# Performance work log

Hardware: AMD Instinct MI355X
Metric: run time of the kernel (lower is better)

## Reference

```python
import jax, jax.numpy as jnp
import numpy as np

N_NODES = 100000
NEG_SLOPE = 0.2  # DGL GATConv default


def gat_layer(x, W, al, ar, src, dst):
    # x: [N, F_in], W: [F_in, H*D], al/ar: [H, D]
    H, D = al.shape
    f = (x @ W).reshape(-1, H, D)                      # [N, H, D]
    el = jnp.einsum('nhd,hd->nh', f, al)               # src attn term
    er = jnp.einsum('nhd,hd->nh', f, ar)               # dst attn term
    e = jax.nn.leaky_relu(el[src] + er[dst], NEG_SLOPE)  # [E, H]
    # segment softmax over incoming edges of each dst node
    m = jax.ops.segment_max(e, dst, num_segments=N_NODES)
    m = jnp.where(jnp.isfinite(m), m, jnp.zeros_like(m))  # isolated nodes -> -inf guard
    ex = jnp.exp(e - m[dst])                           # [E, H]
    s = jax.ops.segment_sum(ex, dst, num_segments=N_NODES)
    alpha = ex / (s[dst] + 1e-9)                       # [E, H]
    msg = f[src] * alpha[:, :, None]                   # [E, H, D]
    out = jax.ops.segment_sum(msg, dst, num_segments=N_NODES)  # [N, H, D]
    return out.reshape(N_NODES, H * D)


def setup_inputs() -> dict:
    key = jax.random.key(0)
    ks = jax.random.split(key, 12)
    x = jax.random.normal(ks[0], (N_NODES, 128), dtype=jnp.float32)
    edge_index = jax.random.randint(ks[1], (2, 1600000), 0, N_NODES, dtype=jnp.int32)
    sc = 0.05
    W0 = jax.random.normal(ks[2], (128, 128), dtype=jnp.float32) * sc
    al0 = jax.random.normal(ks[3], (4, 32), dtype=jnp.float32) * sc
    ar0 = jax.random.normal(ks[4], (4, 32), dtype=jnp.float32) * sc
    W1 = jax.random.normal(ks[5], (128, 128), dtype=jnp.float32) * sc
    al1 = jax.random.normal(ks[6], (4, 32), dtype=jnp.float32) * sc
    ar1 = jax.random.normal(ks[7], (4, 32), dtype=jnp.float32) * sc
    W2 = jax.random.normal(ks[8], (128, 128), dtype=jnp.float32) * sc
    al2 = jax.random.normal(ks[9], (4, 32), dtype=jnp.float32) * sc
    ar2 = jax.random.normal(ks[10], (4, 32), dtype=jnp.float32) * sc
    return {"x": x, "edge_index": edge_index,
            "W0": W0, "al0": al0, "ar0": ar0,
            "W1": W1, "al1": al1, "ar1": ar1,
            "W2": W2, "al2": al2, "ar2": ar2}


def reference(x, edge_index, W0, al0, ar0, W1, al1, ar1, W2, al2, ar2):
    src, dst = edge_index[0], edge_index[1]
    h = x
    for (W, al, ar) in ((W0, al0, ar0), (W1, al1, ar1), (W2, al2, ar2)):
        h = gat_layer(h, W, al, ar, src, dst)
        h = jax.nn.relu(h)  # dropout_rate = 0.0 -> identity
    return h
```

## Files before the change

### kernel.cpp

```cpp
#include <hip/hip_runtime.h>
#include <math.h>

#define NEG_SLOPE 0.2f
#define NBUCK 512
#define BHCHUNK 8192
#define BCHUNK 4096

typedef __attribute__((ext_vector_type(8))) short short8;
typedef __attribute__((ext_vector_type(4))) float f32x4;

__device__ __forceinline__ unsigned short bf16rne(float x) {
    unsigned u = __float_as_uint(x);
    u += 0x7fffu + ((u >> 16) & 1u);
    return (unsigned short)(u >> 16);
}
__device__ __forceinline__ unsigned pack_bf2(float x, float y) {
    unsigned ux = __float_as_uint(x), uy = __float_as_uint(y);
    ux = (ux + 0x7fffu + ((ux >> 16) & 1u)) >> 16;
    uy = (uy + 0x7fffu + ((uy >> 16) & 1u)) & 0xffff0000u;
    return ux | uy;
}

__global__ __launch_bounds__(256) void k_front(
    const int* __restrict__ dst, int* __restrict__ bcnt, int E,
    const float4* __restrict__ x, uint4* __restrict__ Xb, int n8,
    const float* __restrict__ w0, const float* __restrict__ w1,
    const float* __restrict__ w2, unsigned short* __restrict__ Wt,
    int nbB, int nbCvt) {
    __shared__ int cnt[NBUCK];
    int bb = blockIdx.x, t = threadIdx.x;
    if (bb < nbB) {
        for (int i = t; i < NBUCK; i += 256) cnt[i] = 0;
        __syncthreads();
        int e0 = bb * BHCHUNK;
        int n = min(BHCHUNK, E - e0);
        for (int i = t; i < n; i += 256) atomicAdd(&cnt[dst[e0 + i] >> 8], 1);
        __syncthreads();
        for (int i = t; i < NBUCK; i += 256)
            if (cnt[i]) atomicAdd(&bcnt[i], cnt[i]);
    } else if (bb < nbB + nbCvt) {
        int id = (bb - nbB) * 256 + t;
        if (id < n8) {
            float4 a = x[id * 2], b = x[id * 2 + 1];
            uint4 o;
            o.x = pack_bf2(a.x, a.y);
            o.y = pack_bf2(a.z, a.w);
            o.z = pack_bf2(b.x, b.y);
            o.w = pack_bf2(b.z, b.w);
            Xb[id] = o;
        }
    } else {
        int id = (bb - nbB - nbCvt) * 256 + t;
        int layer = id >> 14, rem = id & 16383;
        int k = rem >> 7, n = rem & 127;
        const float* W = (layer == 0) ? w0 : (layer == 1) ? w1 : w2;
        Wt[layer * 16384 + n * 128 + k] = bf16rne(W[k * 128 + n]);
    }
}

__global__ void k_bscan(const int* __restrict__ bcnt, int* __restrict__ bbase,
                        int* __restrict__ bcur, int* __restrict__ rowstart,
                        int N, int E) {
    __shared__ int sd[NBUCK];
    int t = threadIdx.x;
    int c = bcnt[t];
    sd[t] = c;
    __syncthreads();
    for (int s = 1; s < NBUCK; s <<= 1) {
        int x = (t >= s) ? sd[t - s] : 0;
        __syncthreads();
        sd[t] += x;
        __syncthreads();
    }
    int excl = sd[t] - c;
    bbase[t] = excl;
    bcur[t] = excl;
    if (t == NBUCK - 1) bbase[NBUCK] = excl + c;
    if (t == 0) rowstart[N] = E;
}

__global__ __launch_bounds__(256) void k_bin(
    const int* __restrict__ src, const int* __restrict__ dst,
    int* __restrict__ bcur, unsigned* __restrict__ packed, int E) {
    __shared__ int cnt[NBUCK];
    __shared__ int gbase[NBUCK];
    for (int i = threadIdx.x; i < NBUCK; i += 256) cnt[i] = 0;
    __syncthreads();
    int e0 = blockIdx.x * BCHUNK;
    int n = min(BCHUNK, E - e0);
    for (int i = threadIdx.x; i < n; i += 256)
        atomicAdd(&cnt[dst[e0 + i] >> 8], 1);
    __syncthreads();
    for (int i = threadIdx.x; i < NBUCK; i += 256) {
        int c = cnt[i];
        gbase[i] = c ? atomicAdd(&bcur[i], c) : 0;
        cnt[i] = 0;
    }
    __syncthreads();
    for (int i = threadIdx.x; i < n; i += 256) {
        int d = dst[e0 + i];
        int b = d >> 8;
        int o = atomicAdd(&cnt[b], 1);
        packed[gbase[b] + o] = ((unsigned)src[e0 + i] << 8) | (unsigned)(d & 255);
    }
}

__global__ __launch_bounds__(256) void k_place2(
    const unsigned* __restrict__ packed, const int* __restrict__ bbase,
    int* __restrict__ rowstart, unsigned* __restrict__ cpack, int N) {
    __shared__ int cnt[256], sd[256], lcur[256];
    int b = blockIdx.x, t = threadIdx.x;
    int base = bbase[b], end = bbase[b + 1];
    cnt[t] = 0;
    __syncthreads();
    for (int i = base + t; i < end; i += 256)
        atomicAdd(&cnt[packed[i] & 255u], 1);
    __syncthreads();
    sd[t] = cnt[t];
    __syncthreads();
    for (int s = 1; s < 256; s <<= 1) {
        int x = (t >= s) ? sd[t - s] : 0;
        __syncthreads();
        sd[t] += x;
        __syncthreads();
    }
    int excl = sd[t] - cnt[t];
    int gid = (b << 8) + t;
    if (gid < N) rowstart[gid] = base + excl;
    lcur[t] = base + excl;
    __syncthreads();
    for (int i = base + t; i < end; i += 256) {
        unsigned p = packed[i];
        unsigned dl = p & 255u;
        int pos = atomicAdd(&lcur[dl], 1);
        cpack[pos] = (dl << 17) | (p >> 8);
    }
}

__global__ __launch_bounds__(256) void k_gemm(
    const unsigned short* __restrict__ Ab,
    const unsigned short* __restrict__ Wt,
    const float* __restrict__ alv, const float* __restrict__ arv,
    unsigned short* __restrict__ Fb,
    float* __restrict__ el, float* __restrict__ er, int M) {
    __shared__ unsigned short cst[4][32][128];
    int t = threadIdx.x;
    int wv = t >> 6, l = t & 63;
    int l15 = l & 15, quad = l >> 4;
    int row0 = blockIdx.x * 128 + wv * 32;

    f32x4 acc[2][8];
#pragma unroll
    for (int mi = 0; mi < 2; mi++)
#pragma unroll
        for (int nt = 0; nt < 8; nt++)
            acc[mi][nt] = (f32x4){0.f, 0.f, 0.f, 0.f};

    int rA0 = min(row0 + l15, M - 1);
    int rA1 = min(row0 + 16 + l15, M - 1);
    const uint4* pA0 = (const uint4*)(Ab + (size_t)rA0 * 128) + quad;
    const uint4* pA1 = (const uint4*)(Ab + (size_t)rA1 * 128) + quad;
    const uint4* pW = (const uint4*)Wt;

#pragma unroll
    for (int ks = 0; ks < 4; ks++) {
        union { uint4 u; short8 s; } a0, a1, b[8];
        a0.u = pA0[ks * 4];
        a1.u = pA1[ks * 4];
#pragma unroll
        for (int nt = 0; nt < 8; nt++)
            b[nt].u = pW[(nt * 16 + l15) * 16 + quad + ks * 4];
#pragma unroll
        for (int nt = 0; nt < 8; nt++) {
            acc[0][nt] = __builtin_amdgcn_mfma_f32_16x16x32_bf16(a0.s, b[nt].s, acc[0][nt], 0, 0, 0);
            acc[1][nt] = __builtin_amdgcn_mfma_f32_16x16x32_bf16(a1.s, b[nt].s, acc[1][nt], 0, 0, 0);
        }
    }

#pragma unroll
    for (int mi = 0; mi < 2; mi++)
#pragma unroll
        for (int nt = 0; nt < 8; nt++)
#pragma unroll
            for (int r = 0; r < 4; r++)
                cst[wv][mi * 16 + quad * 4 + r][nt * 16 + l15] = bf16rne(acc[mi][nt][r]);

    int rrow = l >> 1;
    int cb = (l & 1) * 64;
    int grow = row0 + rrow;
    bool ok = grow < M;
    float pe[2] = {0.f, 0.f}, pr[2] = {0.f, 0.f};
#pragma unroll
    for (int i = 0; i < 8; i++) {
        uint4 v = *(const uint4*)&cst[wv][rrow][cb + i * 8];
        if (ok) ((uint4*)(Fb + (size_t)grow * 128 + cb))[i] = v;
        int hi = i >> 2;
        int c0 = cb + i * 8;
        unsigned uu[4] = {v.x, v.y, v.z, v.w};
#pragma unroll
        for (int q = 0; q < 4; q++) {
            float fa = __uint_as_float(uu[q] << 16);
            float fb = __uint_as_float(uu[q] & 0xffff0000u);
            pe[hi] += fa * alv[c0 + 2 * q] + fb * alv[c0 + 2 * q + 1];
            pr[hi] += fa * arv[c0 + 2 * q] + fb * arv[c0 + 2 * q + 1];
        }
    }
    float qe0 = __shfl_xor(pe[0], 1, 64), qe1 = __shfl_xor(pe[1], 1, 64);
    float qr0 = __shfl_xor(pr[0], 1, 64), qr1 = __shfl_xor(pr[1], 1, 64);
    if (((l & 1) == 0) && ok) {
        *(float4*)&el[(size_t)grow * 4] = make_float4(pe[0], pe[1], qe0, qe1);
        *(float4*)&er[(size_t)grow * 4] = make_float4(pr[0], pr[1], qr0, qr1);
    }
}

template <int OUT_BF16>
__global__ __launch_bounds__(256) void k_aggr(
    const int* __restrict__ rowstart, const unsigned* __restrict__ cpack,
    const float* __restrict__ el, const float* __restrict__ er,
    const uint4* __restrict__ F4, void* __restrict__ outp, int N, int E) {
    int lane = threadIdx.x & 63;
    int sub = lane >> 4;
    int l16 = lane & 15;
    int h = l16 >> 2;
    int wslot = ((threadIdx.x >> 6) << 2) + sub;

    for (int wbase = blockIdx.x * 16; wbase < N; wbase += gridDim.x * 16) {
        int w = wbase + wslot;
        bool active = w < N;
        int wc = active ? w : N - 1;
        int start = rowstart[wc];
        int dg = active ? (rowstart[wc + 1] - start) : 0;
        float rr = er[(size_t)wc * 4 + h];

        float s_acc = 0.f;
        float a0 = 0.f, a1 = 0.f, a2 = 0.f, a3 = 0.f;
        float a4 = 0.f, a5 = 0.f, a6 = 0.f, a7 = 0.f;

        int ncc = (dg + 3) >> 2;
        int m = max(ncc, __shfl_xor(ncc, 16, 64));
        int nccmax = max(m, __shfl_xor(m, 32, 64));

        auto sload = [&](int c, unsigned* sv) {
            int j = c << 2;
#pragma unroll
            for (int u = 0; u < 4; u++) {
                int e = min(max(start + min(j + u, dg - 1), 0), E - 1);
                sv[u] = cpack[e];
            }
        };
        auto fload = [&](int c, const unsigned* sv, uint4* fb, float* eb) {
            int j = c << 2;
#pragma unroll
            for (int u = 0; u < 4; u++) {
                int s = (int)(sv[u] & 0x1ffffu);
                fb[u] = F4[(size_t)s * 16 + l16];
                float ev = el[(size_t)s * 4 + h];
                eb[u] = (j + u < dg) ? ev : -1e30f;
            }
        };
        auto consume = [&](const uint4* fb, const float* eb) {
#pragma unroll
            for (int u = 0; u < 4; u++) {
                float e = eb[u] + rr;
                e = fmaxf(e, NEG_SLOPE * e);
                float p = __expf(e);
                s_acc += p;
                a0 += p * __uint_as_float(fb[u].x << 16);
                a1 += p * __uint_as_float(fb[u].x & 0xffff0000u);
                a2 += p * __uint_as_float(fb[u].y << 16);
                a3 += p * __uint_as_float(fb[u].y & 0xffff0000u);
                a4 += p * __uint_as_float(fb[u].z << 16);
                a5 += p * __uint_as_float(fb[u].z & 0xffff0000u);
                a6 += p * __uint_as_float(fb[u].w << 16);
                a7 += p * __uint_as_float(fb[u].w & 0xffff0000u);
            }
        };

        unsigned s0[4], s1[4];
        uint4 f0[4], f1[4];
        float e0[4], e1[4];
        if (nccmax > 0) {
            sload(0, s0);
            if (nccmax > 1) sload(1, s1);
            fload(0, s0, f0, e0);
            for (int c = 1; c < nccmax; c++) {
                if (c & 1) {
                    if (c + 1 < nccmax) sload(c + 1, s0);
                    fload(c, s1, f1, e1);
                    consume(f0, e0);
                } else {
                    if (c + 1 < nccmax) sload(c + 1, s1);
                    fload(c, s0, f0, e0);
                    consume(f1, e1);
                }
            }
            if (nccmax & 1) consume(f0, e0); else consume(f1, e1);
        }

        if (active) {
            float inv = 1.f / (s_acc + 1e-9f);
            a0 = fmaxf(a0 * inv, 0.f); a1 = fmaxf(a1 * inv, 0.f);
            a2 = fmaxf(a2 * inv, 0.f); a3 = fmaxf(a3 * inv, 0.f);
            a4 = fmaxf(a4 * inv, 0.f); a5 = fmaxf(a5 * inv, 0.f);
            a6 = fmaxf(a6 * inv, 0.f); a7 = fmaxf(a7 * inv, 0.f);
            if (OUT_BF16) {
                uint4 pk;
                pk.x = pack_bf2(a0, a1);
                pk.y = pack_bf2(a2, a3);
                pk.z = pack_bf2(a4, a5);
                pk.w = pack_bf2(a6, a7);
                ((uint4*)outp)[(size_t)w * 16 + l16] = pk;
            } else {
                float4* op = (float4*)outp + (size_t)w * 32 + l16 * 2;
                op[0] = make_float4(a0, a1, a2, a3);
                op[1] = make_float4(a4, a5, a6, a7);
            }
        }
    }
}


extern "C" void kernel_launch(void* const* d_in, const int* in_sizes, int n_in,
                              void* d_out, int out_size, void* d_ws, size_t ws_size,
                              hipStream_t stream) {
    const float* x = (const float*)d_in[0];
    const int* ei = (const int*)d_in[1];
    int N = in_sizes[0] / 128;
    int E = in_sizes[1] / 2;
    const int* src = ei;
    const int* dst = ei + E;
    const float* Wm[3] = {(const float*)d_in[2], (const float*)d_in[5], (const float*)d_in[8]};
    const float* al[3] = {(const float*)d_in[3], (const float*)d_in[6], (const float*)d_in[9]};
    const float* ar[3] = {(const float*)d_in[4], (const float*)d_in[7], (const float*)d_in[10]};

    char* p = (char*)d_ws;
    auto carve = [&](size_t bytes) {
        char* r = p;
        p += (bytes + 255) & ~(size_t)255;
        return r;
    };
    unsigned short* Xb = (unsigned short*)carve((size_t)N * 128 * 2);
    unsigned short* Hb = (unsigned short*)carve((size_t)N * 128 * 2);
    unsigned short* Fb = (unsigned short*)carve((size_t)N * 128 * 2);
    unsigned short* Wt = (unsigned short*)carve((size_t)3 * 16384 * 2);
    float* el       = (float*)carve((size_t)N * 4 * 4);
    float* er       = (float*)carve((size_t)N * 4 * 4);
    int* rowstart   = (int*)carve((size_t)(N + 1) * 4);
    unsigned* cpack = (unsigned*)carve((size_t)E * 4);
    unsigned* packed= (unsigned*)carve((size_t)E * 4);
    int* bcnt       = (int*)carve((size_t)NBUCK * 4);
    int* bbase      = (int*)carve((size_t)(NBUCK + 1) * 4);
    int* bcur       = (int*)carve((size_t)NBUCK * 4);

    int NBUSED = (N + 255) >> 8;

    hipMemsetAsync(bcnt, 0, NBUCK * 4, stream);
    int nbB = (E + BHCHUNK - 1) / BHCHUNK;
    int n8 = N * 128 / 8;
    int nbCvt = (n8 + 255) / 256;
    int nbPrep = (3 * 16384) / 256;
    k_front<<<nbB + nbCvt + nbPrep, 256, 0, stream>>>(
        dst, bcnt, E, (const float4*)x, (uint4*)Xb, n8,
        Wm[0], Wm[1], Wm[2], Wt, nbB, nbCvt);
    k_bscan<<<1, NBUCK, 0, stream>>>(bcnt, bbase, bcur, rowstart, N, E);
    k_bin<<<(E + BCHUNK - 1) / BCHUNK, 256, 0, stream>>>(src, dst, bcur, packed, E);
    k_place2<<<NBUSED, 256, 0, stream>>>(packed, bbase, rowstart, cpack, N);

    int gb = (N + 127) / 128;
    int ab = min((N + 15) / 16, 2048);
    k_gemm<<<gb, 256, 0, stream>>>(Xb, Wt, al[0], ar[0], Fb, el, er, N);
    k_aggr<1><<<ab, 256, 0, stream>>>(rowstart, cpack, el, er, (const uint4*)Fb, Hb, N, E);

    k_gemm<<<gb, 256, 0, stream>>>(Hb, Wt + 16384, al[1], ar[1], Fb, el, er, N);
    k_aggr<1><<<ab, 256, 0, stream>>>(rowstart, cpack, el, er, (const uint4*)Fb, Hb, N, E);

    k_gemm<<<gb, 256, 0, stream>>>(Hb, Wt + 32768, al[2], ar[2], Fb, el, er, N);
    k_aggr<0><<<ab, 256, 0, stream>>>(rowstart, cpack, el, er, (const uint4*)Fb, d_out, N, E);
}
```

Baseline: 495.8 us.

## Gather neighbor features directly into LDS with double-buffered async loads

After: 493.2 us. No clear change (-0.5%).

```diff
diff --git a/kernel.cpp b/kernel.cpp
--- a/kernel.cpp
+++ b/kernel.cpp
@@ -19,6 +19,12 @@
     ux = (ux + 0x7fffu + ((ux >> 16) & 1u)) >> 16;
     uy = (uy + 0x7fffu + ((uy >> 16) & 1u)) & 0xffff0000u;
     return ux | uy;
+}
+
+__device__ __forceinline__ void gload_lds16(const uint4* g, uint4* l) {
+    __builtin_amdgcn_global_load_lds(
+        (const __attribute__((address_space(1))) void*)g,
+        (__attribute__((address_space(3))) void*)l, 16, 0, 0);
 }
 
 __global__ __launch_bounds__(256) void k_front(
@@ -218,104 +224,124 @@
     const int* __restrict__ rowstart, const unsigned* __restrict__ cpack,
     const float* __restrict__ el, const float* __restrict__ er,
     const uint4* __restrict__ F4, void* __restrict__ outp, int N, int E) {
-    int lane = threadIdx.x & 63;
+    __shared__ uint4 ring[4][2][4][64];
+    int t = threadIdx.x;
+    int wid = t >> 6;
+    int lane = t & 63;
     int sub = lane >> 4;
     int l16 = lane & 15;
     int h = l16 >> 2;
-    int wslot = ((threadIdx.x >> 6) << 2) + sub;
-
-    for (int wbase = blockIdx.x * 16; wbase < N; wbase += gridDim.x * 16) {
-        int w = wbase + wslot;
-        bool active = w < N;
-        int wc = active ? w : N - 1;
-        int start = rowstart[wc];
-        int dg = active ? (rowstart[wc + 1] - start) : 0;
-        float rr = er[(size_t)wc * 4 + h];
-
-        float s_acc = 0.f;
-        float a0 = 0.f, a1 = 0.f, a2 = 0.f, a3 = 0.f;
-        float a4 = 0.f, a5 = 0.f, a6 = 0.f, a7 = 0.f;
-
-        int ncc = (dg + 3) >> 2;
-        int m = max(ncc, __shfl_xor(ncc, 16, 64));
-        int nccmax = max(m, __shfl_xor(m, 32, 64));
-
-        auto sload = [&](int c, unsigned* sv) {
-            int j = c << 2;
-#pragma unroll
-            for (int u = 0; u < 4; u++) {
-                int e = min(max(start + min(j + u, dg - 1), 0), E - 1);
-                sv[u] = cpack[e];
+    int w = blockIdx.x * 16 + (wid << 2) + sub;
+    bool active = w < N;
+    int wc = active ? w : N - 1;
+    int start = rowstart[wc];
+    int dg = active ? (rowstart[wc + 1] - start) : 0;
+    float rr = er[(size_t)wc * 4 + h];
+
+    float s_acc = 0.f;
+    float a0 = 0.f, a1 = 0.f, a2 = 0.f, a3 = 0.f;
+    float a4 = 0.f, a5 = 0.f, a6 = 0.f, a7 = 0.f;
+
+    int ncc = (dg + 3) >> 2;
+    int m = max(ncc, __shfl_xor(ncc, 16, 64));
+    int nccmax = max(m, __shfl_xor(m, 32, 64));
+
+    auto sload = [&](int c, unsigned* sv) {
+        int j = c << 2;
+#pragma unroll
+        for (int u = 0; u < 4; u++) {
+            int e = max(start + min(j + u, dg - 1), 0);
+            sv[u] = cpack[e];
+        }
+    };
+    auto eload = [&](int c, const unsigned* sv, float* ebuf) {
+        int j = c << 2;
+#pragma unroll
+        for (int u = 0; u < 4; u++) {
+            int s = (int)(sv[u] & 0x1ffffu);
+            float ev = el[(size_t)s * 4 + h];
+            ebuf[u] = (j + u < dg) ? ev : -1e30f;
+        }
+    };
+    auto gissue = [&](const unsigned* sv, uint4* dst) {
+#pragma unroll
+        for (int u = 0; u < 4; u++) {
+            int s = (int)(sv[u] & 0x1ffffu);
+            gload_lds16(F4 + (size_t)s * 16 + l16, dst + u * 64);
+        }
+    };
+    auto consume = [&](const uint4* base, const float* ebuf) {
+#pragma unroll
+        for (int u = 0; u < 4; u++) {
+            uint4 f = base[u * 64 + lane];
+            float e = ebuf[u] + rr;
+            e = fmaxf(e, NEG_SLOPE * e);
+            float p = __expf(e);
+            s_acc += p;
+            a0 += p * __uint_as_float(f.x << 16);
+            a1 += p * __uint_as_float(f.x & 0xffff0000u);
+            a2 += p * __uint_as_float(f.y << 16);
+            a3 += p * __uint_as_float(f.y & 0xffff0000u);
+            a4 += p * __uint_as_float(f.z << 16);
+            a5 += p * __uint_as_float(f.z & 0xffff0000u);
+            a6 += p * __uint_as_float(f.w << 16);
+            a7 += p * __uint_as_float(f.w & 0xffff0000u);
+        }
+    };
+
+    unsigned svA[4], svB[4];
+    float ebA[4], ebB[4];
+    uint4* slot0 = &ring[wid][0][0][0];
+    uint4* slot1 = &ring[wid][1][0][0];
+    if (nccmax > 0) {
+        sload(0, svA);
+        if (nccmax > 1) sload(1, svB);
+        eload(0, svA, ebA);
+        gissue(svA, slot0);
+        int c = 0;
+        for (;;) {
+            if (c + 1 < nccmax) {
+                eload(c + 1, svB, ebB);
+                if (c + 2 < nccmax) sload(c + 2, svA);
+                gissue(svB, slot1);
+                asm volatile("s_waitcnt vmcnt(4)" ::: "memory");
+            } else {
+                asm volatile("s_waitcnt vmcnt(0)" ::: "memory");
             }
-        };
-        auto fload = [&](int c, const unsigned* sv, uint4* fb, float* eb) {
-            int j = c << 2;
-#pragma unroll
-            for (int u = 0; u < 4; u++) {
-                int s = (int)(sv[u] & 0x1ffffu);
-                fb[u] = F4[(size_t)s * 16 + l16];
-                float ev = el[(size_t)s * 4 + h];
-                eb[u] = (j + u < dg) ? ev : -1e30f;
+            __builtin_amdgcn_sched_barrier(0);
+            consume(slot0, ebA);
+            if (++c >= nccmax) break;
+            if (c + 1 < nccmax) {
+                eload(c + 1, svA, ebA);
+                if (c + 2 < nccmax) sload(c + 2, svB);
+                gissue(svA, slot0);
+                asm volatile("s_waitcnt vmcnt(4)" ::: "memory");
+            } else {
+                asm volatile("s_waitcnt vmcnt(0)" ::: "memory");
             }
-        };
-        auto consume = [&](const uint4* fb, const float* eb) {
-#pragma unroll
-            for (int u = 0; u < 4; u++) {
-                float e = eb[u] + rr;
-                e = fmaxf(e, NEG_SLOPE * e);
-                float p = __expf(e);
-                s_acc += p;
-                a0 += p * __uint_as_float(fb[u].x << 16);
-                a1 += p * __uint_as_float(fb[u].x & 0xffff0000u);
-                a2 += p * __uint_as_float(fb[u].y << 16);
-                a3 += p * __uint_as_float(fb[u].y & 0xffff0000u);
-                a4 += p * __uint_as_float(fb[u].z << 16);
-                a5 += p * __uint_as_float(fb[u].z & 0xffff0000u);
-                a6 += p * __uint_as_float(fb[u].w << 16);
-                a7 += p * __uint_as_float(fb[u].w & 0xffff0000u);
-            }
-        };
-
-        unsigned s0[4], s1[4];
-        uint4 f0[4], f1[4];
-        float e0[4], e1[4];
-        if (nccmax > 0) {
-            sload(0, s0);
-            if (nccmax > 1) sload(1, s1);
-            fload(0, s0, f0, e0);
-            for (int c = 1; c < nccmax; c++) {
-                if (c & 1) {
-                    if (c + 1 < nccmax) sload(c + 1, s0);
-                    fload(c, s1, f1, e1);
-                    consume(f0, e0);
-                } else {
-                    if (c + 1 < nccmax) sload(c + 1, s1);
-                    fload(c, s0, f0, e0);
-                    consume(f1, e1);
-                }
-            }
-            if (nccmax & 1) consume(f0, e0); else consume(f1, e1);
-        }
-
-        if (active) {
-            float inv = 1.f / (s_acc + 1e-9f);
-            a0 = fmaxf(a0 * inv, 0.f); a1 = fmaxf(a1 * inv, 0.f);
-            a2 = fmaxf(a2 * inv, 0.f); a3 = fmaxf(a3 * inv, 0.f);
-            a4 = fmaxf(a4 * inv, 0.f); a5 = fmaxf(a5 * inv, 0.f);
-            a6 = fmaxf(a6 * inv, 0.f); a7 = fmaxf(a7 * inv, 0.f);
-            if (OUT_BF16) {
-                uint4 pk;
-                pk.x = pack_bf2(a0, a1);
-                pk.y = pack_bf2(a2, a3);
-                pk.z = pack_bf2(a4, a5);
-                pk.w = pack_bf2(a6, a7);
-                ((uint4*)outp)[(size_t)w * 16 + l16] = pk;
-            } else {
-                float4* op = (float4*)outp + (size_t)w * 32 + l16 * 2;
-                op[0] = make_float4(a0, a1, a2, a3);
-                op[1] = make_float4(a4, a5, a6, a7);
-            }
-        }
+            __builtin_amdgcn_sched_barrier(0);
+            consume(slot1, ebB);
+            if (++c >= nccmax) break;
+        }
+    }
+
+    if (!active) return;
+    float inv = 1.f / (s_acc + 1e-9f);
+    a0 = fmaxf(a0 * inv, 0.f); a1 = fmaxf(a1 * inv, 0.f);
+    a2 = fmaxf(a2 * inv, 0.f); a3 = fmaxf(a3 * inv, 0.f);
+    a4 = fmaxf(a4 * inv, 0.f); a5 = fmaxf(a5 * inv, 0.f);
+    a6 = fmaxf(a6 * inv, 0.f); a7 = fmaxf(a7 * inv, 0.f);
+    if (OUT_BF16) {
+        uint4 pk;
+        pk.x = pack_bf2(a0, a1);
+        pk.y = pack_bf2(a2, a3);
+        pk.z = pack_bf2(a4, a5);
+        pk.w = pack_bf2(a6, a7);
+        ((uint4*)outp)[(size_t)w * 16 + l16] = pk;
+    } else {
+        float4* op = (float4*)outp + (size_t)w * 32 + l16 * 2;
+        op[0] = make_float4(a0, a1, a2, a3);
+        op[1] = make_float4(a4, a5, a6, a7);
     }
 }
 
@@ -367,7 +393,7 @@
     k_place2<<<NBUSED, 256, 0, stream>>>(packed, bbase, rowstart, cpack, N);
 
     int gb = (N + 127) / 128;
-    int ab = min((N + 15) / 16, 2048);
+    int ab = (N + 15) / 16;
     k_gemm<<<gb, 256, 0, stream>>>(Xb, Wt, al[0], ar[0], Fb, el, er, N);
     k_aggr<1><<<ab, 256, 0, stream>>>(rowstart, cpack, el, er, (const uint4*)Fb, Hb, N, E);
 
```
